# Kernel optimization log

Hardware: AMD Instinct MI355X
Metric: run time of the kernel (lower is better)

## Reference

```python
import jax, jax.numpy as jnp
import numpy as np

C = 768      # token feature dim
N = 196      # tokens per stream
R_DIM = 2 * 2 * N  # 784 = concat(A row, A col)


def setup_inputs() -> dict:
    key = jax.random.key(0)
    ks = jax.random.split(key, 16)
    s = 1.0 / np.sqrt(C)
    inp = {
        "x": jax.random.normal(ks[0], (128, N, C), dtype=jnp.float32),
        "y": jax.random.normal(ks[1], (128, N, C), dtype=jnp.float32),
        # linear_conv_1: 1x1 conv (768->768) + BN affine (eval) + ReLU
        "W1": jax.random.normal(ks[2], (C, C), dtype=jnp.float32) * s,
        "b1": jnp.zeros((C,), dtype=jnp.float32),
        "g1": jax.random.uniform(ks[3], (C,), dtype=jnp.float32, minval=0.5, maxval=1.5),
        "be1": jax.random.normal(ks[4], (C,), dtype=jnp.float32) * 0.1,
        # linear_conv_2
        "W2": jax.random.normal(ks[5], (C, C), dtype=jnp.float32) * s,
        "b2": jnp.zeros((C,), dtype=jnp.float32),
        "g2": jax.random.uniform(ks[6], (C,), dtype=jnp.float32, minval=0.5, maxval=1.5),
        "be2": jax.random.normal(ks[7], (C,), dtype=jnp.float32) * 0.1,
        # linear_conv_3: 768->768
        "W3": jax.random.normal(ks[8], (C, C), dtype=jnp.float32) * s,
        "b3": jnp.zeros((C,), dtype=jnp.float32),
        # linear_conv_4: 784->784 over relation rows
        "W4": jax.random.normal(ks[9], (784, 784), dtype=jnp.float32) / np.sqrt(784.0),
        "b4": jnp.zeros((784,), dtype=jnp.float32),
        # linear_conv_5: (768+784)->1
        "W5": jax.random.normal(ks[10], (C + 784, 1), dtype=jnp.float32) / np.sqrt(C + 784.0),
        "b5": jnp.zeros((1,), dtype=jnp.float32),
    }
    return inp


def reference(x, y, W1, b1, g1, be1, W2, b2, g2, be2, W3, b3, W4, b4, W5, b5):
    # per-token 1x1 conv + BN(eval)->affine + ReLU
    phi_x = jax.nn.relu((x @ W1 + b1) * g1 + be1)          # [B,196,768]
    phi_y = jax.nn.relu((y @ W2 + b2) * g2 + be2)          # [B,196,768]
    cat_phi = jnp.concatenate([phi_x, phi_y], axis=1)      # [B,392,768]
    # affinity matrix A = cat_phi @ cat_phi^T
    A = jnp.einsum("bnd,bmd->bnm", cat_phi, cat_phi)       # [B,392,392]
    # R[i] = concat(A[i,:], A[:,i]) -> vectorized as [A | A^T]
    R = jnp.concatenate([A, jnp.swapaxes(A, 1, 2)], axis=2)  # [B,392,784]
    v = cat_phi @ W3 + b3                                   # [B,392,768]
    v_ = R @ W4 + b4                                        # [B,392,784]
    cat_v = jnp.concatenate([v, v_], axis=2)                # [B,392,1552]
    W = cat_v @ W5 + b5                                     # [B,392,1]
    # per-token reweighting then sum of the two streams
    out = x * W[:, :N, :] + y * W[:, N:, :]                 # [B,196,768]
    return out
```

## Files before the change

kernel.cpp:

```cpp
#include <hip/hip_runtime.h>

typedef __bf16 bf16_t;
typedef bf16_t bf16x8 __attribute__((ext_vector_type(8)));
typedef float f32x4 __attribute__((ext_vector_type(4)));
typedef float f32x16 __attribute__((ext_vector_type(16)));
typedef unsigned short u16x8 __attribute__((ext_vector_type(8)));
typedef unsigned short u16x4 __attribute__((ext_vector_type(4)));

#define CD 768
#define NT 196
#define NB 128
#define T2 392
#define MROWS (NB*NT)
#define NTILE 1176

__device__ __forceinline__ unsigned short f2bf(float f){
  unsigned u = __float_as_uint(f);
  u += 0x7fffu + ((u >> 16) & 1u);
  return (unsigned short)(u >> 16);
}
__device__ __forceinline__ float bf2f(unsigned short h){
  return __uint_as_float(((unsigned)h) << 16);
}
__device__ __forceinline__ float wave_reduce(float v){
  #pragma unroll
  for (int o = 32; o > 0; o >>= 1) v += __shfl_down(v, o, 64);
  return v;
}
__device__ __forceinline__ void gload16(const unsigned short* g, unsigned short* l){
  __builtin_amdgcn_global_load_lds(
      (const __attribute__((address_space(1))) unsigned int*)g,
      (__attribute__((address_space(3))) unsigned int*)l, 16, 0, 0);
}

__global__ __launch_bounds__(256) void prep_wt(const float* __restrict__ W1,
                        const float* __restrict__ W2,
                        unsigned short* __restrict__ W1t, unsigned short* __restrict__ W2t){
  __shared__ float tile[64][65];
  const float* src = blockIdx.z ? W2 : W1;
  unsigned short* dst = blockIdx.z ? W2t : W1t;
  int k0 = blockIdx.x*64, n0 = blockIdx.y*64;
  int tid = threadIdx.x;
  #pragma unroll
  for (int e = 0; e < 16; ++e){
    int idx = e*256 + tid;
    int r = idx >> 6, c = idx & 63;
    tile[r][c] = src[(size_t)(k0+r)*CD + n0 + c];
  }
  __syncthreads();
  #pragma unroll
  for (int e = 0; e < 16; ++e){
    int idx = e*256 + tid;
    int nr = idx >> 6, kc = idx & 63;
    dst[(size_t)(n0+nr)*CD + k0 + kc] = f2bf(tile[kc][nr]);
  }
}

__global__ void prep_u(const float* __restrict__ W3, const float* __restrict__ W4,
                       const float* __restrict__ W5, const float* __restrict__ b3,
                       const float* __restrict__ b4, const float* __restrict__ b5,
                       float* __restrict__ u3, float* __restrict__ u4s, float* __restrict__ cbuf){
  int wid = (blockIdx.x*blockDim.x + threadIdx.x) >> 6;
  int lane = threadIdx.x & 63;
  const float* w5a = W5;
  const float* w5b = W5 + CD;
  float s = 0.f;
  if (wid < CD){
    const float* row = W3 + (size_t)wid*CD;
    for (int k = lane; k < CD; k += 64) s += row[k]*w5a[k];
    s = wave_reduce(s);
    if (lane == 0) u3[wid] = s;
  } else if (wid < CD + T2){
    int j = wid - CD;
    const float* r0 = W4 + (size_t)j*784;
    const float* r1 = W4 + (size_t)(j+T2)*784;
    for (int e = lane; e < 784; e += 64) s += (r0[e]+r1[e])*w5b[e];
    s = wave_reduce(s);
    if (lane == 0) u4s[j] = s;
  } else if (wid == CD + T2){
    for (int k = lane; k < CD; k += 64) s += b3[k]*w5a[k];
    for (int e = lane; e < 784; e += 64) s += b4[e]*w5b[e];
    s = wave_reduce(s);
    if (lane == 0) cbuf[0] = s + b5[0];
  }
}

__global__ void init_t(const float* __restrict__ u3, float* __restrict__ t){
  int i = blockIdx.x*256 + threadIdx.x;
  if (i < (NB+2)*CD) t[i] = (i < NB*CD) ? u3[i % CD] : 0.f;
}

__global__ __launch_bounds__(256) void cvt2(const float* __restrict__ x,
                                            const float* __restrict__ y,
                                            unsigned short* __restrict__ dst){
  const int nv = MROWS*CD/8;
  for (int id = blockIdx.x*256 + threadIdx.x; id < 2*nv; id += gridDim.x*256){
    const float* s = (id < nv) ? x : y;
    int i = (id < nv) ? id : id - nv;
    float4 a = ((const float4*)s)[i*2];
    float4 b = ((const float4*)s)[i*2+1];
    u16x8 o = { f2bf(a.x), f2bf(a.y), f2bf(a.z), f2bf(a.w),
                f2bf(b.x), f2bf(b.y), f2bf(b.z), f2bf(b.w) };
    ((u16x8*)dst)[id] = o;
  }
}

__global__ __launch_bounds__(256, 4) void phi_gemm2(
    const unsigned short* __restrict__ Ax, const unsigned short* __restrict__ Ay,
    const unsigned short* __restrict__ Bx, const unsigned short* __restrict__ By,
    const float* __restrict__ biasX, const float* __restrict__ gamX, const float* __restrict__ betX,
    const float* __restrict__ biasY, const float* __restrict__ gamY, const float* __restrict__ betY,
    const float* __restrict__ u4s,
    unsigned short* __restrict__ Px, unsigned short* __restrict__ Py,
    float* __restrict__ t, int mode)
{
  __shared__ unsigned short As[128*64];
  __shared__ unsigned short Bs[128*64];

  const int tid  = threadIdx.x;
  const int lane = tid & 63;
  const int w    = tid >> 6;
  const int wr = w >> 1, wc = w & 1;

  const int chunk = gridDim.x >> 3;
  int orig = blockIdx.x;
  int swz  = (orig & 7)*chunk + (orig >> 3);
  int s, r;
  if (mode < 0){ s = swz >= NTILE; r = swz - s*NTILE; }
  else         { s = mode; r = swz; }
  const int bn = r % 6;
  const int bm = r / 6;

  const unsigned short* A   = s ? Ay : Ax;
  const unsigned short* Bt  = s ? By : Bx;
  const float* bias = s ? biasY : biasX;
  const float* gam  = s ? gamY  : gamX;
  const float* bet  = s ? betY  : betX;
  const float* u4c  = u4s + s*NT;
  unsigned short* phi = s ? Py : Px;

  const int srow = lane >> 3;
  const int p    = lane & 7;
  const int g0   = (p - srow) & 7;
  const unsigned short* a0 = A  + (size_t)(bm*128 + w*32 + srow)*CD + g0*8;
  const unsigned short* b0 = Bt + (size_t)(bn*128 + w*32 + srow)*CD + g0*8;
  unsigned short* al = &As[(w*32)*64];
  unsigned short* bl = &Bs[(w*32)*64];

  const int l31 = lane & 31;
  const int lh  = lane >> 5;
  const int r7  = l31 & 7;

  f32x16 acc[2][2] = {};

  #pragma unroll 1
  for (int kt = 0; kt < 12; ++kt){
    const int ko = kt*64;
    #pragma unroll
    for (int c = 0; c < 4; ++c){
      gload16(a0 + (size_t)c*8*CD + ko, al + c*512);
      gload16(b0 + (size_t)c*8*CD + ko, bl + c*512);
    }
    __syncthreads();
    #pragma unroll
    for (int ks = 0; ks < 4; ++ks){
      const int phys = ((ks*2 + lh) + r7) & 7;
      bf16x8 af[2], bq[2];
      #pragma unroll
      for (int mi = 0; mi < 2; ++mi){
        int rr = wr*64 + mi*32 + l31;
        af[mi] = *(const bf16x8*)(&As[rr*64 + phys*8]);
      }
      #pragma unroll
      for (int nj = 0; nj < 2; ++nj){
        int cc = wc*64 + nj*32 + l31;
        bq[nj] = *(const bf16x8*)(&Bs[cc*64 + phys*8]);
      }
      #pragma unroll
      for (int mi = 0; mi < 2; ++mi)
        #pragma unroll
        for (int nj = 0; nj < 2; ++nj)
          acc[mi][nj] = __builtin_amdgcn_mfma_f32_32x32x16_bf16(af[mi], bq[nj], acc[mi][nj], 0, 0, 0);
    }
    if (kt < 11) __syncthreads();
  }

  const int b_base = (bm*128) / NT;
  int  col0 = bn*128 + wc*64 + l31;
  float bi0 = bias[col0],    ga0 = gam[col0],    be0 = bet[col0];
  float bi1 = bias[col0+32], ga1 = gam[col0+32], be1 = bet[col0+32];
  float cb[2][2] = {{0.f,0.f},{0.f,0.f}};
  #pragma unroll
  for (int mi = 0; mi < 2; ++mi){
    #pragma unroll
    for (int reg = 0; reg < 16; ++reg){
      int rg  = bm*128 + wr*64 + mi*32 + (reg & 3) + 8*(reg >> 2) + 4*lh;
      int b   = rg / NT;
      int tok = rg - b*NT;
      float uw = u4c[tok];
      int bk  = b - b_base;
      #pragma unroll
      for (int nj = 0; nj < 2; ++nj){
        float v = (nj ? (acc[mi][nj][reg] + bi1)*ga1 + be1
                      : (acc[mi][nj][reg] + bi0)*ga0 + be0);
        v = fmaxf(v, 0.f);
        phi[(size_t)rg*CD + col0 + nj*32] = f2bf(v);
        float pv = uw*v;
        cb[nj][0] += (bk == 0) ? pv : 0.f;
        cb[nj][1] += (bk == 1) ? pv : 0.f;
      }
    }
  }
  #pragma unroll
  for (int nj = 0; nj < 2; ++nj){
    cb[nj][0] += __shfl_xor(cb[nj][0], 32, 64);
    cb[nj][1] += __shfl_xor(cb[nj][1], 32, 64);
  }
  if (lane < 32){
    atomicAdd(&t[(size_t)(b_base  )*CD + col0   ], cb[0][0]);
    atomicAdd(&t[(size_t)(b_base+1)*CD + col0   ], cb[0][1]);
    atomicAdd(&t[(size_t)(b_base  )*CD + col0+32], cb[1][0]);
    atomicAdd(&t[(size_t)(b_base+1)*CD + col0+32], cb[1][1]);
  }
}

template<bool USEBF>
__global__ __launch_bounds__(256) void comp_wout(
    const unsigned short* __restrict__ phiX, const unsigned short* __restrict__ phiY,
    const float* __restrict__ t, const float* __restrict__ cbuf,
    const float* __restrict__ x, const float* __restrict__ y,
    const unsigned short* __restrict__ xb, const unsigned short* __restrict__ yb,
    float* __restrict__ out)
{
  int gw   = (blockIdx.x*256 + threadIdx.x) >> 6;
  int lane = threadIdx.x & 63;
  int b = gw / NT;
  const unsigned short* px = phiX + (size_t)gw*CD;
  const unsigned short* py = phiY + (size_t)gw*CD;
  const float* tb = t + (size_t)b*CD;
  float s1 = 0.f, s2 = 0.f;
  #pragma unroll
  for (int it = 0; it < 3; ++it){
    int k = it*256 + lane*4;
    float4 tv = *(const float4*)(tb + k);
    u16x4 ux = *(const u16x4*)(px + k);
    u16x4 uy = *(const u16x4*)(py + k);
    s1 += bf2f(ux.x)*tv.x + bf2f(ux.y)*tv.y + bf2f(ux.z)*tv.z + bf2f(ux.w)*tv.w;
    s2 += bf2f(uy.x)*tv.x + bf2f(uy.y)*tv.y + bf2f(uy.z)*tv.z + bf2f(uy.w)*tv.w;
  }
  s1 = wave_reduce(s1);
  s2 = wave_reduce(s2);
  float cc = cbuf[0];
  float wx = __shfl(s1, 0, 64) + cc;
  float wy = __shfl(s2, 0, 64) + cc;
  float* orow = out + (size_t)gw*CD;
  #pragma unroll
  for (int it = 0; it < 3; ++it){
    int k = it*256 + lane*4;
    float4 xv, yv;
    if (USEBF){
      u16x4 a  = *(const u16x4*)(xb + (size_t)gw*CD + k);
      u16x4 c4 = *(const u16x4*)(yb + (size_t)gw*CD + k);
      xv = float4{bf2f(a.x), bf2f(a.y), bf2f(a.z), bf2f(a.w)};
      yv = float4{bf2f(c4.x), bf2f(c4.y), bf2f(c4.z), bf2f(c4.w)};
    } else {
      xv = *(const float4*)(x + (size_t)gw*CD + k);
      yv = *(const float4*)(y + (size_t)gw*CD + k);
    }
    float4 o;
    o.x = xv.x*wx + yv.x*wy;
    o.y = xv.y*wx + yv.y*wy;
    o.z = xv.z*wx + yv.z*wy;
    o.w = xv.w*wx + yv.w*wy;
    *(float4*)(orow + k) = o;
  }
}

extern "C" void kernel_launch(void* const* d_in, const int* in_sizes, int n_in,
                              void* d_out, int out_size, void* d_ws, size_t ws_size,
                              hipStream_t stream){
  const float* x  = (const float*)d_in[0];
  const float* y  = (const float*)d_in[1];
  const float* W1 = (const float*)d_in[2];
  const float* b1 = (const float*)d_in[3];
  const float* g1 = (const float*)d_in[4];
  const float* be1= (const float*)d_in[5];
  const float* W2 = (const float*)d_in[6];
  const float* b2 = (const float*)d_in[7];
  const float* g2 = (const float*)d_in[8];
  const float* be2= (const float*)d_in[9];
  const float* W3 = (const float*)d_in[10];
  const float* b3 = (const float*)d_in[11];
  const float* W4 = (const float*)d_in[12];
  const float* b4 = (const float*)d_in[13];
  const float* W5 = (const float*)d_in[14];
  const float* b5 = (const float*)d_in[15];
  float* out = (float*)d_out;

  const size_t BIGE = (size_t)MROWS*CD;
  const size_t smallF = CD + T2 + 4 + (size_t)(NB+2)*CD;
  const size_t need4 = (2*(size_t)CD*CD + 4*BIGE)*2 + smallF*4 + 256;
  const bool big = (ws_size >= need4);

  unsigned short* W1t = (unsigned short*)d_ws;
  unsigned short* W2t = W1t + CD*CD;
  unsigned short* Sx  = W2t + CD*CD;
  unsigned short* Sy  = Sx + BIGE;
  unsigned short* Px, * Py;
  float* smalls;
  if (big){
    Px = Sy + BIGE;
    Py = Px + BIGE;
    smalls = (float*)(Py + BIGE);
  } else {
    Px = Sy + BIGE;
    Py = Sx;
    smalls = (float*)(Px + BIGE);
  }
  float* u3   = smalls;
  float* u4s  = u3 + CD;
  float* cbuf = u4s + T2;
  float* t    = cbuf + 4;

  prep_wt<<<dim3(12,12,2), 256, 0, stream>>>(W1, W2, W1t, W2t);
  prep_u<<<(CD + T2 + 4)/4, 256, 0, stream>>>(W3, W4, W5, b3, b4, b5, u3, u4s, cbuf);
  init_t<<<((NB+2)*CD + 255)/256, 256, 0, stream>>>(u3, t);

  cvt2<<<2048, 256, 0, stream>>>(x, y, Sx);

  if (big){
    phi_gemm2<<<2*NTILE, 256, 0, stream>>>(Sx, Sy, W1t, W2t,
        b1, g1, be1, b2, g2, be2, u4s, Px, Py, t, -1);
    comp_wout<true><<<MROWS/4, 256, 0, stream>>>(Px, Py, t, cbuf, x, y, Sx, Sy, out);
  } else {
    phi_gemm2<<<NTILE, 256, 0, stream>>>(Sx, Sy, W1t, W2t,
        b1, g1, be1, b2, g2, be2, u4s, Px, Py, t, 0);
    phi_gemm2<<<NTILE, 256, 0, stream>>>(Sx, Sy, W1t, W2t,
        b1, g1, be1, b2, g2, be2, u4s, Px, Py, t, 1);
    comp_wout<false><<<MROWS/4, 256, 0, stream>>>(Px, Py, t, cbuf, x, y, Sx, Sy, out);
  }
}
```

Measured before the change: 180.1 us.

## Pre-pack weights in MFMA fragment order and load B directly to registers

The weight transpose kernel is replaced by a packing kernel that writes W1/W2 in the per-lane MFMA operand layout (32-column groups by k-step). The GEMM then loads B fragments straight from global memory into registers, skipping the B shared-memory tile. This halves LDS usage and LDS reads, which may raise occupancy. In exchange, each wave issues its own B global loads without cross-wave sharing, and those loads are exposed before the barrier.

```diff
diff --git a/kernel.cpp b/kernel.cpp
--- a/kernel.cpp
+++ b/kernel.cpp
@@ -33,27 +33,26 @@
       (__attribute__((address_space(3))) unsigned int*)l, 16, 0, 0);
 }
 
-__global__ __launch_bounds__(256) void prep_wt(const float* __restrict__ W1,
+__global__ __launch_bounds__(256) void prep_pack(const float* __restrict__ W1,
                         const float* __restrict__ W2,
-                        unsigned short* __restrict__ W1t, unsigned short* __restrict__ W2t){
-  __shared__ float tile[64][65];
+                        unsigned short* __restrict__ W1p, unsigned short* __restrict__ W2p){
+  __shared__ float tile[64][33];
   const float* src = blockIdx.z ? W2 : W1;
-  unsigned short* dst = blockIdx.z ? W2t : W1t;
-  int k0 = blockIdx.x*64, n0 = blockIdx.y*64;
-  int tid = threadIdx.x;
-  #pragma unroll
-  for (int e = 0; e < 16; ++e){
+  unsigned short* dst = blockIdx.z ? W2p : W1p;
+  const int kt = blockIdx.x, g = blockIdx.y, tid = threadIdx.x;
+  #pragma unroll
+  for (int e = 0; e < 8; ++e){
     int idx = e*256 + tid;
-    int r = idx >> 6, c = idx & 63;
-    tile[r][c] = src[(size_t)(k0+r)*CD + n0 + c];
+    int kk = idx >> 5, nn = idx & 31;
+    tile[kk][nn] = src[(size_t)(kt*64 + kk)*CD + g*32 + nn];
   }
   __syncthreads();
-  #pragma unroll
-  for (int e = 0; e < 16; ++e){
-    int idx = e*256 + tid;
-    int nr = idx >> 6, kc = idx & 63;
-    dst[(size_t)(n0+nr)*CD + k0 + kc] = f2bf(tile[kc][nr]);
-  }
+  const int ks = tid >> 6, lane = tid & 63;
+  const int l31 = lane & 31, lh = lane >> 5;
+  unsigned short* o = dst + ((size_t)((g*12 + kt)*4 + ks)*64 + lane)*8;
+  #pragma unroll
+  for (int i = 0; i < 8; ++i)
+    o[i] = f2bf(tile[ks*16 + lh*8 + i][l31]);
 }
 
 __global__ void prep_u(const float* __restrict__ W3, const float* __restrict__ W4,
@@ -107,7 +106,7 @@
 
 __global__ __launch_bounds__(256, 4) void phi_gemm2(
     const unsigned short* __restrict__ Ax, const unsigned short* __restrict__ Ay,
-    const unsigned short* __restrict__ Bx, const unsigned short* __restrict__ By,
+    const unsigned short* __restrict__ W1p, const unsigned short* __restrict__ W2p,
     const float* __restrict__ biasX, const float* __restrict__ gamX, const float* __restrict__ betX,
     const float* __restrict__ biasY, const float* __restrict__ gamY, const float* __restrict__ betY,
     const float* __restrict__ u4s,
@@ -115,7 +114,6 @@
     float* __restrict__ t, int mode)
 {
   __shared__ unsigned short As[128*64];
-  __shared__ unsigned short Bs[128*64];
 
   const int tid  = threadIdx.x;
   const int lane = tid & 63;
@@ -132,7 +130,7 @@
   const int bm = r / 6;
 
   const unsigned short* A   = s ? Ay : Ax;
-  const unsigned short* Bt  = s ? By : Bx;
+  const unsigned short* Wp  = s ? W2p : W1p;
   const float* bias = s ? biasY : biasX;
   const float* gam  = s ? gamY  : gamX;
   const float* bet  = s ? betY  : betX;
@@ -142,10 +140,11 @@
   const int srow = lane >> 3;
   const int p    = lane & 7;
   const int g0   = (p - srow) & 7;
-  const unsigned short* a0 = A  + (size_t)(bm*128 + w*32 + srow)*CD + g0*8;
-  const unsigned short* b0 = Bt + (size_t)(bn*128 + w*32 + srow)*CD + g0*8;
+  const unsigned short* a0 = A + (size_t)(bm*128 + w*32 + srow)*CD + g0*8;
   unsigned short* al = &As[(w*32)*64];
-  unsigned short* bl = &Bs[(w*32)*64];
+
+  const unsigned short* bb0 = Wp + ((size_t)(bn*4 + wc*2    )*48)*512 + lane*8;
+  const unsigned short* bb1 = Wp + ((size_t)(bn*4 + wc*2 + 1)*48)*512 + lane*8;
 
   const int l31 = lane & 31;
   const int lh  = lane >> 5;
@@ -157,30 +156,29 @@
   for (int kt = 0; kt < 12; ++kt){
     const int ko = kt*64;
     #pragma unroll
-    for (int c = 0; c < 4; ++c){
+    for (int c = 0; c < 4; ++c)
       gload16(a0 + (size_t)c*8*CD + ko, al + c*512);
-      gload16(b0 + (size_t)c*8*CD + ko, bl + c*512);
+    bf16x8 bq[2][4];
+    #pragma unroll
+    for (int ks = 0; ks < 4; ++ks){
+      bq[0][ks] = *(const bf16x8*)(bb0 + (kt*4 + ks)*512);
+      bq[1][ks] = *(const bf16x8*)(bb1 + (kt*4 + ks)*512);
     }
     __syncthreads();
     #pragma unroll
     for (int ks = 0; ks < 4; ++ks){
       const int phys = ((ks*2 + lh) + r7) & 7;
-      bf16x8 af[2], bq[2];
+      bf16x8 af[2];
       #pragma unroll
       for (int mi = 0; mi < 2; ++mi){
         int rr = wr*64 + mi*32 + l31;
         af[mi] = *(const bf16x8*)(&As[rr*64 + phys*8]);
       }
       #pragma unroll
-      for (int nj = 0; nj < 2; ++nj){
-        int cc = wc*64 + nj*32 + l31;
-        bq[nj] = *(const bf16x8*)(&Bs[cc*64 + phys*8]);
-      }
-      #pragma unroll
       for (int mi = 0; mi < 2; ++mi)
         #pragma unroll
         for (int nj = 0; nj < 2; ++nj)
-          acc[mi][nj] = __builtin_amdgcn_mfma_f32_32x32x16_bf16(af[mi], bq[nj], acc[mi][nj], 0, 0, 0);
+          acc[mi][nj] = __builtin_amdgcn_mfma_f32_32x32x16_bf16(af[mi], bq[nj][ks], acc[mi][nj], 0, 0, 0);
     }
     if (kt < 11) __syncthreads();
   }
@@ -302,9 +300,9 @@
   const size_t need4 = (2*(size_t)CD*CD + 4*BIGE)*2 + smallF*4 + 256;
   const bool big = (ws_size >= need4);
 
-  unsigned short* W1t = (unsigned short*)d_ws;
-  unsigned short* W2t = W1t + CD*CD;
-  unsigned short* Sx  = W2t + CD*CD;
+  unsigned short* W1p = (unsigned short*)d_ws;
+  unsigned short* W2p = W1p + CD*CD;
+  unsigned short* Sx  = W2p + CD*CD;
   unsigned short* Sy  = Sx + BIGE;
   unsigned short* Px, * Py;
   float* smalls;
@@ -322,20 +320,20 @@
   float* cbuf = u4s + T2;
   float* t    = cbuf + 4;
 
-  prep_wt<<<dim3(12,12,2), 256, 0, stream>>>(W1, W2, W1t, W2t);
+  prep_pack<<<dim3(12,24,2), 256, 0, stream>>>(W1, W2, W1p, W2p);
   prep_u<<<(CD + T2 + 4)/4, 256, 0, stream>>>(W3, W4, W5, b3, b4, b5, u3, u4s, cbuf);
   init_t<<<((NB+2)*CD + 255)/256, 256, 0, stream>>>(u3, t);
 
   cvt2<<<2048, 256, 0, stream>>>(x, y, Sx);
 
   if (big){
-    phi_gemm2<<<2*NTILE, 256, 0, stream>>>(Sx, Sy, W1t, W2t,
+    phi_gemm2<<<2*NTILE, 256, 0, stream>>>(Sx, Sy, W1p, W2p,
         b1, g1, be1, b2, g2, be2, u4s, Px, Py, t, -1);
     comp_wout<true><<<MROWS/4, 256, 0, stream>>>(Px, Py, t, cbuf, x, y, Sx, Sy, out);
   } else {
-    phi_gemm2<<<NTILE, 256, 0, stream>>>(Sx, Sy, W1t, W2t,
+    phi_gemm2<<<NTILE, 256, 0, stream>>>(Sx, Sy, W1p, W2p,
         b1, g1, be1, b2, g2, be2, u4s, Px, Py, t, 0);
-    phi_gemm2<<<NTILE, 256, 0, stream>>>(Sx, Sy, W1t, W2t,
+    phi_gemm2<<<NTILE, 256, 0, stream>>>(Sx, Sy, W1p, W2p,
         b1, g1, be1, b2, g2, be2, u4s, Px, Py, t, 1);
     comp_wout<false><<<MROWS/4, 256, 0, stream>>>(Px, Py, t, cbuf, x, y, Sx, Sy, out);
   }
```

New measurement: 181.5 us. Within noise of the previous version (+0.8%).

## Warp-specialize phi GEMM into producer and consumer waves with double-buffered LDS

Applied to the files above, without the earlier changes.

The phi GEMM block grows from 256 to 512 threads. Four producer waves stream the next K tile into a second LDS buffer while four consumer waves run MFMAs on the current buffer, with one barrier per iteration. This is meant to hide global-load latency behind compute. In exchange, LDS use doubles to 64KB per block and half the waves do no math, which may lower occupancy. There is also a risk that the producer waves' early return interacts badly with any barrier in the epilogue.

```diff
diff --git a/kernel.cpp b/kernel.cpp
--- a/kernel.cpp
+++ b/kernel.cpp
@@ -105,7 +105,7 @@
   }
 }
 
-__global__ __launch_bounds__(256, 4) void phi_gemm2(
+__global__ __launch_bounds__(512, 4) void phi_gemm2(
     const unsigned short* __restrict__ Ax, const unsigned short* __restrict__ Ay,
     const unsigned short* __restrict__ Bx, const unsigned short* __restrict__ By,
     const float* __restrict__ biasX, const float* __restrict__ gamX, const float* __restrict__ betX,
@@ -114,13 +114,16 @@
     unsigned short* __restrict__ Px, unsigned short* __restrict__ Py,
     float* __restrict__ t, int mode)
 {
-  __shared__ unsigned short As[128*64];
-  __shared__ unsigned short Bs[128*64];
+  __shared__ unsigned short As[2][128*64];
+  __shared__ unsigned short Bs[2][128*64];
 
   const int tid  = threadIdx.x;
   const int lane = tid & 63;
   const int w    = tid >> 6;
-  const int wr = w >> 1, wc = w & 1;
+  const bool producer = (w < 4);
+  const int pw = w;
+  const int cw = w & 3;
+  const int wr = cw >> 1, wc = cw & 1;
 
   const int chunk = gridDim.x >> 3;
   int orig = blockIdx.x;
@@ -142,10 +145,8 @@
   const int srow = lane >> 3;
   const int p    = lane & 7;
   const int g0   = (p - srow) & 7;
-  const unsigned short* a0 = A  + (size_t)(bm*128 + w*32 + srow)*CD + g0*8;
-  const unsigned short* b0 = Bt + (size_t)(bn*128 + w*32 + srow)*CD + g0*8;
-  unsigned short* al = &As[(w*32)*64];
-  unsigned short* bl = &Bs[(w*32)*64];
+  const unsigned short* a0 = A  + (size_t)(bm*128 + pw*32 + srow)*CD + g0*8;
+  const unsigned short* b0 = Bt + (size_t)(bn*128 + pw*32 + srow)*CD + g0*8;
 
   const int l31 = lane & 31;
   const int lh  = lane >> 5;
@@ -153,37 +154,46 @@
 
   f32x16 acc[2][2] = {};
 
+#define STAGE(D, KT) { const int ko = (KT)*64;                         \
+    _Pragma("unroll")                                                  \
+    for (int c = 0; c < 4; ++c){                                       \
+      gload16(a0 + (size_t)c*8*CD + ko, &As[D][pw*2048 + c*512]);      \
+      gload16(b0 + (size_t)c*8*CD + ko, &Bs[D][pw*2048 + c*512]); } }
+
+#define COMPUTE(D) {                                                   \
+    _Pragma("unroll")                                                  \
+    for (int ks = 0; ks < 4; ++ks){                                    \
+      const int phys = ((ks*2 + lh) + r7) & 7;                         \
+      bf16x8 af[2], bq[2];                                             \
+      _Pragma("unroll")                                                \
+      for (int mi = 0; mi < 2; ++mi){ int rr = wr*64 + mi*32 + l31;    \
+        af[mi] = *(const bf16x8*)(&As[D][rr*64 + phys*8]); }           \
+      _Pragma("unroll")                                                \
+      for (int nj = 0; nj < 2; ++nj){ int cc = wc*64 + nj*32 + l31;    \
+        bq[nj] = *(const bf16x8*)(&Bs[D][cc*64 + phys*8]); }           \
+      _Pragma("unroll")                                                \
+      for (int mi = 0; mi < 2; ++mi)                                   \
+        _Pragma("unroll")                                              \
+        for (int nj = 0; nj < 2; ++nj)                                 \
+          acc[mi][nj] = __builtin_amdgcn_mfma_f32_32x32x16_bf16(af[mi], bq[nj], acc[mi][nj], 0, 0, 0); } }
+
+  if (producer) STAGE(0, 0)
+  __syncthreads();
+
   #pragma unroll 1
   for (int kt = 0; kt < 12; ++kt){
-    const int ko = kt*64;
-    #pragma unroll
-    for (int c = 0; c < 4; ++c){
-      gload16(a0 + (size_t)c*8*CD + ko, al + c*512);
-      gload16(b0 + (size_t)c*8*CD + ko, bl + c*512);
+    const int D = kt & 1;
+    if (producer){
+      if (kt < 11) STAGE(D^1, kt+1)
+    } else {
+      COMPUTE(D)
     }
     __syncthreads();
-    #pragma unroll
-    for (int ks = 0; ks < 4; ++ks){
-      const int phys = ((ks*2 + lh) + r7) & 7;
-      bf16x8 af[2], bq[2];
-      #pragma unroll
-      for (int mi = 0; mi < 2; ++mi){
-        int rr = wr*64 + mi*32 + l31;
-        af[mi] = *(const bf16x8*)(&As[rr*64 + phys*8]);
-      }
-      #pragma unroll
-      for (int nj = 0; nj < 2; ++nj){
-        int cc = wc*64 + nj*32 + l31;
-        bq[nj] = *(const bf16x8*)(&Bs[cc*64 + phys*8]);
-      }
-      #pragma unroll
-      for (int mi = 0; mi < 2; ++mi)
-        #pragma unroll
-        for (int nj = 0; nj < 2; ++nj)
-          acc[mi][nj] = __builtin_amdgcn_mfma_f32_32x32x16_bf16(af[mi], bq[nj], acc[mi][nj], 0, 0, 0);
-    }
-    if (kt < 11) __syncthreads();
-  }
+  }
+#undef COMPUTE
+#undef STAGE
+
+  if (producer) return;
 
   const int b_base = (bm*128) / NT;
   int  col0 = bn*128 + wc*64 + l31;
@@ -329,13 +339,13 @@
   cvt2<<<2048, 256, 0, stream>>>(x, y, Sx);
 
   if (big){
-    phi_gemm2<<<2*NTILE, 256, 0, stream>>>(Sx, Sy, W1t, W2t,
+    phi_gemm2<<<2*NTILE, 512, 0, stream>>>(Sx, Sy, W1t, W2t,
         b1, g1, be1, b2, g2, be2, u4s, Px, Py, t, -1);
     comp_wout<true><<<MROWS/4, 256, 0, stream>>>(Px, Py, t, cbuf, x, y, Sx, Sy, out);
   } else {
-    phi_gemm2<<<NTILE, 256, 0, stream>>>(Sx, Sy, W1t, W2t,
+    phi_gemm2<<<NTILE, 512, 0, stream>>>(Sx, Sy, W1t, W2t,
         b1, g1, be1, b2, g2, be2, u4s, Px, Py, t, 0);
-    phi_gemm2<<<NTILE, 256, 0, stream>>>(Sx, Sy, W1t, W2t,
+    phi_gemm2<<<NTILE, 512, 0, stream>>>(Sx, Sy, W1t, W2t,
         b1, g1, be1, b2, g2, be2, u4s, Px, Py, t, 1);
     comp_wout<false><<<MROWS/4, 256, 0, stream>>>(Px, Py, t, cbuf, x, y, Sx, Sy, out);
   }
```

New measurement: 179.5 us. No clear change (-0.3%).
